# Kernel tuning notes

Hardware: AMD Instinct MI355X
Metric: run time of the kernel (lower is better)

Reference implementation:

```python
import jax, jax.numpy as jnp
import numpy as np

N = 8192
HID = 256
NCLS = 5
K = 10  # adj_parameter
IN_DIMS = [1000, 1000, 503]


def _leaky(x):
    return jnp.where(x >= 0, x, 0.25 * x)


def _batchnorm(x, g, b):
    # training-mode BatchNorm1d with batch stats (biased var), eps=1e-5
    mu = jnp.mean(x, axis=0)
    var = jnp.mean((x - mu) ** 2, axis=0)
    return (x - mu) * jax.lax.rsqrt(var + 1e-5) * g + b


def _build_adj(feat):
    # cosine similarity, per-row top-(K+1) (top-1 is self, diag=1), scatter,
    # add identity, L1 row-normalize. Vectorized equivalent of the torch loop.
    norm = jnp.maximum(jnp.linalg.norm(feat, axis=1, keepdims=True), 1e-12)
    fn = feat / norm
    sim = fn @ fn.T                                  # [N, N]
    vals, idx = jax.lax.top_k(sim, K + 1)            # [N, K+1]
    rows = jnp.arange(sim.shape[0])[:, None]
    adj = jnp.zeros_like(sim).at[rows, idx[:, 1:]].set(vals[:, 1:])
    adj = adj + jnp.eye(sim.shape[0], dtype=sim.dtype)
    rs = jnp.maximum(jnp.sum(jnp.abs(adj), axis=1, keepdims=True), 1e-12)
    return adj / rs


def setup_inputs() -> dict:
    key = jax.random.key(0)
    ks = jax.random.split(key, 24)
    d = {}
    d['x1'] = jax.random.normal(ks[0], (N, IN_DIMS[0]), jnp.float32)
    d['x2'] = jax.random.normal(ks[1], (N, IN_DIMS[1]), jnp.float32)
    d['x3'] = jax.random.normal(ks[2], (N, IN_DIMS[2]), jnp.float32)
    def xavier(k, shape):
        fan_in, fan_out = shape[-2], shape[-1]
        std = np.sqrt(2.0 / (fan_in + fan_out))
        return jax.random.normal(k, shape, jnp.float32) * std
    d['enc_W1'] = xavier(ks[3], (IN_DIMS[0], HID))
    d['enc_W2'] = xavier(ks[4], (IN_DIMS[1], HID))
    d['enc_W3'] = xavier(ks[5], (IN_DIMS[2], HID))
    d['enc_b'] = jnp.zeros((3, HID), jnp.float32)
    d['bn_g'] = jnp.ones((3, HID), jnp.float32)
    d['bn_b'] = jnp.zeros((3, HID), jnp.float32)
    d['gc1_W'] = xavier(ks[6], (3, HID, HID))
    d['gc1_b'] = jnp.zeros((3, HID), jnp.float32)
    d['gc2_W'] = xavier(ks[7], (3, HID, HID))
    d['gc2_b'] = jnp.zeros((3, HID), jnp.float32)
    d['clf_W'] = xavier(ks[8], (3, HID, NCLS))
    d['clf_b'] = jnp.zeros((3, NCLS), jnp.float32)
    d['attn'] = xavier(ks[9], (3, 1))[:, 0]
    d['f1_W'] = xavier(ks[10], (NCLS, 128))
    d['f1_b'] = jnp.zeros((128,), jnp.float32)
    d['f2_W'] = xavier(ks[11], (128, NCLS))
    d['f2_b'] = jnp.zeros((NCLS,), jnp.float32)
    return d


def reference(x1, x2, x3, enc_W1, enc_W2, enc_W3, enc_b, bn_g, bn_b,
              gc1_W, gc1_b, gc2_W, gc2_b, clf_W, clf_b,
              attn, f1_W, f1_b, f2_W, f2_b):
    xs = [x1, x2, x3]
    enc_Ws = [enc_W1, enc_W2, enc_W3]
    logits_list = []
    for i in range(3):
        # modal encoder: Linear -> ReLU -> BatchNorm (dropout off, eval)
        feat = jax.nn.relu(xs[i] @ enc_Ws[i] + enc_b[i])
        feat = _batchnorm(feat, bn_g[i], bn_b[i])
        adj = _build_adj(feat)
        # SimpleGCN: two GraphConvolution layers with leaky_relu(0.25)
        h = _leaky(adj @ (feat @ gc1_W[i]) + gc1_b[i])
        h = _leaky(adj @ (h @ gc2_W[i]) + gc2_b[i])
        logits_list.append(h @ clf_W[i] + clf_b[i])
    # SimpleVCDN fusion
    w = jax.nn.softmax(attn)
    fused = sum(w[i] * jax.nn.sigmoid(logits_list[i]) for i in range(3))
    out = _leaky(fused @ f1_W + f1_b) @ f2_W + f2_b
    return out
```

## Files before the change

### kernel.cpp

```cpp
#include <hip/hip_runtime.h>
#include <cfloat>
#include <cstdint>
#include <cstddef>

#define NROWS 8192
#define HID 256
#define NCLS 5
#define TOPK 10
#define CAP 256
#define TM 128
#define TN 128
#define BK 32
#define BKS 64

typedef __bf16 bf16x8 __attribute__((ext_vector_type(8)));
typedef float f32x4 __attribute__((ext_vector_type(4)));

__device__ inline ushort f2bf(float x) {
  unsigned u = __float_as_uint(x);
  unsigned r = (u + 0x7fffu + ((u >> 16) & 1u)) >> 16;
  return (ushort)r;
}
__device__ inline float bf2f(ushort b) { return __uint_as_float(((unsigned)b) << 16); }

__device__ __forceinline__ void load_lds16(const void* g, void* l) {
  __builtin_amdgcn_global_load_lds(
      (const __attribute__((address_space(1))) void*)g,
      (__attribute__((address_space(3))) void*)l, 16, 0, 0);
}

__global__ __launch_bounds__(256) void packAB_kernel(const float* __restrict__ X0,
    const float* __restrict__ X1, const float* __restrict__ X2,
    const float* __restrict__ W0, const float* __restrict__ W1,
    const float* __restrict__ W2, ushort* __restrict__ Ah, ushort* __restrict__ Al,
    ushort* __restrict__ Bh, ushort* __restrict__ Bl,
    int D0, int D1, int D2, int Kp0, int Kp1, int Kp2,
    size_t aOff0, size_t aOff1, size_t aOff2,
    size_t wOff0, size_t wOff1, size_t wOff2) {
  const int z = blockIdx.y;
  const float* X = (z == 0) ? X0 : (z == 1) ? X1 : X2;
  const float* W = (z == 0) ? W0 : (z == 1) ? W1 : W2;
  const int D = (z == 0) ? D0 : (z == 1) ? D1 : D2;
  const int Kp = (z == 0) ? Kp0 : (z == 1) ? Kp1 : Kp2;
  const size_t aOff = (z == 0) ? aOff0 : (z == 1) ? aOff1 : aOff2;
  const size_t wOff = (z == 0) ? wOff0 : (z == 1) ? wOff1 : wOff2;
  const int ksh = 31 - __clz(Kp);
  const int id = blockIdx.x * 256 + threadIdx.x;
  const int atotal = NROWS << ksh;
  if (id >= atotal + (HID << ksh)) return;
  if (id < atotal) {
    const int k = id & (Kp - 1);
    const int r = id >> ksh;
    const float x = (k < D) ? X[(size_t)r * D + k] : 0.f;
    const ushort h = f2bf(x);
    Ah[aOff + id] = h;
    Al[aOff + id] = f2bf(x - bf2f(h));
  } else {
    const int id2 = id - atotal;
    const int k = id2 & (Kp - 1);
    const int n = id2 >> ksh;
    const float x = (k < D) ? W[(size_t)k * HID + n] : 0.f;
    const ushort h = f2bf(x);
    Bh[wOff + id2] = h;
    Bl[wOff + id2] = f2bf(x - bf2f(h));
  }
}

__global__ __launch_bounds__(256) void packW_kernel(const float* __restrict__ W,
    ushort* __restrict__ Bh, ushort* __restrict__ Bl) {
  const int z = blockIdx.y;
  const int id = blockIdx.x * 256 + threadIdx.x;
  const int k = id >> 8, n = id & 255;
  const size_t wz = (size_t)z * HID * HID;
  const float x = W[wz + (size_t)k * HID + n];
  const ushort h = f2bf(x);
  Bh[wz + (size_t)n * HID + k] = h;
  Bl[wz + (size_t)n * HID + k] = f2bf(x - bf2f(h));
}

template<bool BIAS, int ACT>
__global__ __launch_bounds__(256) void limbgemm_kernel(const ushort* __restrict__ Ah,
    const ushort* __restrict__ Al, const ushort* __restrict__ Bh,
    const ushort* __restrict__ Bl, const float* __restrict__ bias,
    float* __restrict__ C, int Kp0, int Kp1, int Kp2,
    size_t aOff0, size_t aOff1, size_t aOff2,
    size_t bOff0, size_t bOff1, size_t bOff2) {
  __shared__ ushort AsH[TM * BK], AsL[TM * BK], BsH[TM * BK], BsL[TM * BK];
  const int z = blockIdx.y;
  const int Kp = (z == 0) ? Kp0 : (z == 1) ? Kp1 : Kp2;
  const size_t aO = (z == 0) ? aOff0 : (z == 1) ? aOff1 : aOff2;
  const size_t bO = (z == 0) ? bOff0 : (z == 1) ? bOff1 : bOff2;
  Ah += aO; Al += aO; Bh += bO; Bl += bO;
  C += (size_t)z * NROWS * HID;
  const int tid = threadIdx.x;
  const int wave = tid >> 6, lane = tid & 63;
  const int bid = blockIdx.x;
  const int xcd = bid & 7, slot = bid >> 3;
  const int bxi = slot & 1;
  const int byi = xcd * 8 + (slot >> 1);
  const int bm = byi * TM, bn = bxi * 128;
  const int wr = (wave >> 1) * 64, wc = (wave & 1) * 64;

  f32x4 acc[4][4];
  const f32x4 zero = {0.f, 0.f, 0.f, 0.f};
  #pragma unroll
  for (int i = 0; i < 4; ++i)
    #pragma unroll
    for (int j = 0; j < 4; ++j) acc[i][j] = zero;

  const int p0 = tid, p1 = tid + 256;
  const int r0 = p0 >> 2, kl0 = (p0 & 3) ^ ((r0 & 3) ^ ((r0 >> 2) & 1));
  const int r1 = p1 >> 2, kl1 = (p1 & 3) ^ ((r1 & 3) ^ ((r1 >> 2) & 1));
  const size_t a0 = (size_t)(bm + r0) * Kp + kl0 * 8;
  const size_t a1 = (size_t)(bm + r1) * Kp + kl1 * 8;
  const size_t b0 = (size_t)(bn + r0) * Kp + kl0 * 8;
  const size_t b1 = (size_t)(bn + r1) * Kp + kl1 * 8;

  for (int k0 = 0; k0 < Kp; k0 += BK) {
    __syncthreads();
    load_lds16(Ah + a0 + k0, &AsH[p0 * 8]);
    load_lds16(Ah + a1 + k0, &AsH[p1 * 8]);
    load_lds16(Al + a0 + k0, &AsL[p0 * 8]);
    load_lds16(Al + a1 + k0, &AsL[p1 * 8]);
    load_lds16(Bh + b0 + k0, &BsH[p0 * 8]);
    load_lds16(Bh + b1 + k0, &BsH[p1 * 8]);
    load_lds16(Bl + b0 + k0, &BsL[p0 * 8]);
    load_lds16(Bl + b1 + k0, &BsL[p1 * 8]);
    __syncthreads();
    bf16x8 ah[4], al[4], bh[4], bl[4];
    const int kg = lane >> 4;
    #pragma unroll
    for (int f = 0; f < 4; ++f) {
      const int m = wr + f * 16 + (lane & 15);
      const int sa = m * 4 + (kg ^ (m & 3) ^ ((m >> 2) & 1));
      ah[f] = *(const bf16x8*)&AsH[sa * 8];
      al[f] = *(const bf16x8*)&AsL[sa * 8];
      const int n = wc + f * 16 + (lane & 15);
      const int sb = n * 4 + (kg ^ (n & 3) ^ ((n >> 2) & 1));
      bh[f] = *(const bf16x8*)&BsH[sb * 8];
      bl[f] = *(const bf16x8*)&BsL[sb * 8];
    }
    #pragma unroll
    for (int fr = 0; fr < 4; ++fr)
      #pragma unroll
      for (int fc = 0; fc < 4; ++fc) {
        acc[fr][fc] = __builtin_amdgcn_mfma_f32_16x16x32_bf16(ah[fr], bh[fc], acc[fr][fc], 0, 0, 0);
        acc[fr][fc] = __builtin_amdgcn_mfma_f32_16x16x32_bf16(ah[fr], bl[fc], acc[fr][fc], 0, 0, 0);
        acc[fr][fc] = __builtin_amdgcn_mfma_f32_16x16x32_bf16(al[fr], bh[fc], acc[fr][fc], 0, 0, 0);
      }
  }
  const int cq = lane >> 4, cc = lane & 15;
  #pragma unroll
  for (int fr = 0; fr < 4; ++fr) {
    #pragma unroll
    for (int fc = 0; fc < 4; ++fc) {
      const int rb = bm + wr + fr * 16 + cq * 4;
      const int col = bn + wc + fc * 16 + cc;
      const float bb = BIAS ? bias[z * HID + col] : 0.f;
      float* cp = C + (size_t)rb * HID + col;
      #pragma unroll
      for (int e = 0; e < 4; ++e) {
        float v = acc[fr][fc][e] + bb;
        if (ACT == 1) v = fmaxf(v, 0.f);
        cp[(size_t)e * HID] = v;
      }
    }
  }
}

__global__ __launch_bounds__(256) void bn_stats_kernel(const float* __restrict__ F,
    float* __restrict__ ps, float* __restrict__ ps2) {
  const int z = blockIdx.y;
  const int b = blockIdx.x, t = threadIdx.x;
  float s = 0.f, s2 = 0.f;
  const float* p = F + (size_t)z * NROWS * HID + (size_t)b * 128 * HID + t;
  for (int r = 0; r < 128; ++r) {
    const float v = p[(size_t)r * HID];
    s += v; s2 += v * v;
  }
  ps[(size_t)z * 64 * HID + b * HID + t] = s;
  ps2[(size_t)z * 64 * HID + b * HID + t] = s2;
}

__global__ __launch_bounds__(256) void bn_finalize_kernel(const float* __restrict__ ps,
    const float* __restrict__ ps2, const float* __restrict__ g,
    const float* __restrict__ b, float* __restrict__ scale, float* __restrict__ shift) {
  const int z = blockIdx.x;
  const int t = threadIdx.x;
  float s = 0.f, s2 = 0.f;
  for (int i = 0; i < 64; ++i) {
    s += ps[(size_t)z * 64 * HID + i * HID + t];
    s2 += ps2[(size_t)z * 64 * HID + i * HID + t];
  }
  const float mu = s / (float)NROWS;
  const float var = s2 / (float)NROWS - mu * mu;
  const float rstd = rsqrtf(var + 1e-5f);
  const float sc = rstd * g[z * HID + t];
  scale[z * HID + t] = sc;
  shift[z * HID + t] = b[z * HID + t] - mu * sc;
}

__global__ __launch_bounds__(256) void bn_rownorm_kernel(const float* __restrict__ F,
    const float* __restrict__ scale, const float* __restrict__ shift,
    float* __restrict__ FN, ushort* __restrict__ Ph,
    ushort* __restrict__ Fh, ushort* __restrict__ Fl) {
  const int z = blockIdx.y;
  const int r = blockIdx.x, t = threadIdx.x;
  const size_t zb = (size_t)z * NROWS * HID;
  const float f = F[zb + (size_t)r * HID + t] * scale[z * HID + t] + shift[z * HID + t];
  __shared__ float sh[256];
  sh[t] = f * f;
  __syncthreads();
  for (int st = 128; st > 0; st >>= 1) {
    if (t < st) sh[t] += sh[t + st];
    __syncthreads();
  }
  const float inv = 1.0f / fmaxf(sqrtf(sh[0]), 1e-12f);
  const float fn = f * inv;
  const size_t o = zb + (size_t)r * HID + t;
  FN[o] = fn;
  Ph[o] = f2bf(fn);
  const ushort h = f2bf(f);
  Fh[o] = h;
  Fl[o] = f2bf(f - bf2f(h));
}

template<int PASS>
__global__ __launch_bounds__(512) void simtile_kernel(const ushort* __restrict__ P,
    float* __restrict__ M, const float* __restrict__ tauv,
    int* __restrict__ gcnt, int* __restrict__ gidx) {
  const int bx = blockIdx.x, by = blockIdx.y;
  if (by > bx) return;
  const int z = blockIdx.z;
  P += (size_t)z * NROWS * HID;
  if (PASS == 0) M += (size_t)z * NROWS * 64;
  else {
    tauv += (size_t)z * NROWS;
    gcnt += (size_t)z * NROWS;
    gidx += (size_t)z * NROWS * CAP;
  }
  const bool offdiag = (bx != by);
  __shared__ ushort As[TM * BKS];
  __shared__ ushort Bs[TN * BKS];
  __shared__ float Ml[2][TM];
  __shared__ float MlC[4][TN];
  __shared__ float taulA[TM];
  __shared__ float taulB[TN];
  const int tid = threadIdx.x;
  const int wave = tid >> 6, lane = tid & 63;
  const int bm = by * TM;
  const int bn = bx * TN;
  const int wr = (wave >> 1) * 32;
  const int wc = (wave & 1) * 64;

  if (PASS == 1) {
    if (tid < TM) taulA[tid] = tauv[bm + tid];
    else if (tid < TM + TN) taulB[tid - TM] = tauv[bn + (tid - TM)];
  }

  const ushort* pa[2];
  const ushort* pb[2];
  #pragma unroll
  for (int j = 0; j < 2; ++j) {
    const int s = tid + j * 512;
    const int m = s >> 3;
    const int kg = (s & 7) ^ (m & 7);
    pa[j] = P + (size_t)(bm + m) * HID + kg * 8;
    pb[j] = P + (size_t)(bn + m) * HID + kg * 8;
  }

  f32x4 acc[2][4];
  const f32x4 zero = {0.f, 0.f, 0.f, 0.f};
  #pragma unroll
  for (int i = 0; i < 2; ++i)
    #pragma unroll
    for (int j = 0; j < 4; ++j) acc[i][j] = zero;

  for (int k0 = 0; k0 < HID; k0 += BKS) {
    __syncthreads();
    #pragma unroll
    for (int j = 0; j < 2; ++j) {
      load_lds16(pa[j] + k0, &As[(tid + j * 512) * 8]);
      load_lds16(pb[j] + k0, &Bs[(tid + j * 512) * 8]);
    }
    __syncthreads();
    #pragma unroll
    for (int h = 0; h < 2; ++h) {
      const int kgb = h * 4 + (lane >> 4);
      bf16x8 af[2], bf[4];
      #pragma unroll
      for (int f = 0; f < 2; ++f) {
        const int m = wr + f * 16 + (lane & 15);
        const int sa = m * 8 + (kgb ^ (m & 7));
        af[f] = *(const bf16x8*)&As[sa * 8];
      }
      #pragma unroll
      for (int f = 0; f < 4; ++f) {
        const int n = wc + f * 16 + (lane & 15);
        const int sb = n * 8 + (kgb ^ (n & 7));
        bf[f] = *(const bf16x8*)&Bs[sb * 8];
      }
      #pragma unroll
      for (int fr = 0; fr < 2; ++fr)
        #pragma unroll
        for (int fc = 0; fc < 4; ++fc)
          acc[fr][fc] = __builtin_amdgcn_mfma_f32_16x16x32_bf16(af[fr], bf[fc], acc[fr][fc], 0, 0, 0);
    }
  }

  const int cq = lane >> 4, cc = lane & 15;
  if (PASS == 0) {
    #pragma unroll
    for (int fr = 0; fr < 2; ++fr) {
      #pragma unroll
      for (int e = 0; e < 4; ++e) {
        const int lrow = wr + fr * 16 + cq * 4 + e;
        const int grow = bm + lrow;
        float mx = -FLT_MAX;
        #pragma unroll
        for (int fc = 0; fc < 4; ++fc) {
          const int col = bn + wc + fc * 16 + cc;
          mx = fmaxf(mx, (col == grow) ? -FLT_MAX : acc[fr][fc][e]);
        }
        #pragma unroll
        for (int s = 1; s < 16; s <<= 1) mx = fmaxf(mx, __shfl_xor(mx, s));
        if (cc == 0) Ml[wave & 1][lrow] = mx;
      }
    }
    if (offdiag) {
      #pragma unroll
      for (int fc = 0; fc < 4; ++fc) {
        float mx = -FLT_MAX;
        #pragma unroll
        for (int fr = 0; fr < 2; ++fr)
          #pragma unroll
          for (int e = 0; e < 4; ++e) mx = fmaxf(mx, acc[fr][fc][e]);
        mx = fmaxf(mx, __shfl_xor(mx, 16));
        mx = fmaxf(mx, __shfl_xor(mx, 32));
        if (cq == 0) MlC[wave >> 1][wc + fc * 16 + cc] = mx;
      }
    }
    __syncthreads();
    if (tid < TM) M[(size_t)(bm + tid) * 64 + bx] = fmaxf(Ml[0][tid], Ml[1][tid]);
    if (offdiag && tid < TN) {
      const float mx = fmaxf(fmaxf(MlC[0][tid], MlC[1][tid]),
                             fmaxf(MlC[2][tid], MlC[3][tid]));
      M[(size_t)(bn + tid) * 64 + by] = mx;
    }
  } else {
    __syncthreads();
    #pragma unroll
    for (int fr = 0; fr < 2; ++fr) {
      #pragma unroll
      for (int e = 0; e < 4; ++e) {
        const int lrow = wr + fr * 16 + cq * 4 + e;
        const int grow = bm + lrow;
        const float tA = taulA[lrow];
        #pragma unroll
        for (int fc = 0; fc < 4; ++fc) {
          const int lcol = wc + fc * 16 + cc;
          const int gcol = bn + lcol;
          const float v = acc[fr][fc][e];
          if (gcol != grow && v >= tA) {
            const int pos = atomicAdd(&gcnt[grow], 1);
            if (pos < CAP) gidx[(size_t)grow * CAP + pos] = gcol;
          }
          if (offdiag && v >= taulB[lcol]) {
            const int pos = atomicAdd(&gcnt[gcol], 1);
            if (pos < CAP) gidx[(size_t)gcol * CAP + pos] = grow;
          }
        }
      }
    }
  }
}

__global__ __launch_bounds__(256) void tau_kernel(const float* __restrict__ M,
    float* __restrict__ tauv, int* __restrict__ gcnt) {
  const int z = blockIdx.y;
  const int wave = threadIdx.x >> 6, lane = threadIdx.x & 63;
  const int row = blockIdx.x * 4 + wave;
  float cur = M[(size_t)z * NROWS * 64 + (size_t)row * 64 + lane];
  float tau = cur;
  #pragma unroll
  for (int sel = 0; sel < 16; ++sel) {
    float bv = cur;
    int bl = lane;
    #pragma unroll
    for (int s = 1; s < 64; s <<= 1) {
      const float ov = __shfl_xor(bv, s);
      const int ol = __shfl_xor(bl, s);
      if (ov > bv || (ov == bv && ol < bl)) { bv = ov; bl = ol; }
    }
    tau = bv;
    if (lane == bl) cur = -FLT_MAX;
  }
  if (lane == 0) {
    tauv[(size_t)z * NROWS + row] = tau;
    gcnt[(size_t)z * NROWS + row] = 0;
  }
}

__global__ __launch_bounds__(256) void refine_kernel(const int* __restrict__ gcnt,
    const int* __restrict__ gidx, const float* __restrict__ FN,
    int* __restrict__ nidx, float* __restrict__ nval, float* __restrict__ dinv) {
  const int z = blockIdx.y;
  gcnt += (size_t)z * NROWS;
  gidx += (size_t)z * NROWS * CAP;
  FN += (size_t)z * NROWS * HID;
  nidx += (size_t)z * NROWS * TOPK;
  nval += (size_t)z * NROWS * TOPK;
  dinv += (size_t)z * NROWS;
  const int wave = threadIdx.x >> 6, lane = threadIdx.x & 63;
  const int row = blockIdx.x * 4 + wave;
  const int cnt = min(gcnt[row], CAP);
  __shared__ float fnrow[4][HID];
  __shared__ float ev[4][CAP];
  ((float4*)fnrow[wave])[lane] = ((const float4*)(FN + (size_t)row * HID))[lane];
  __syncthreads();
  const int c = lane >> 2, q4 = lane & 3;
  for (int b0 = 0; b0 < cnt; b0 += 16) {
    const int ci = b0 + c;
    const int cand = (ci < cnt) ? gidx[(size_t)row * CAP + ci] : 0;
    float s = 0.f;
    const float* fc = FN + (size_t)cand * HID + q4 * 64;
    const float* fr = fnrow[wave] + q4 * 64;
    #pragma unroll 8
    for (int k = 0; k < 64; ++k) s += fr[k] * fc[k];
    s += __shfl_xor(s, 1);
    s += __shfl_xor(s, 2);
    if (q4 == 0 && ci < cnt) ev[wave][ci] = s;
  }
  __syncthreads();
  float outv[TOPK];
  int outi[TOPK];
  float sum = 1.0f;
  #pragma unroll
  for (int sel = 0; sel < TOPK; ++sel) {
    float bv = -FLT_MAX;
    int bp = 0;
    #pragma unroll
    for (int j = 0; j < 4; ++j) {
      const int p = lane + j * 64;
      if (p < cnt) {
        const float v = ev[wave][p];
        if (v > bv) { bv = v; bp = p; }
      }
    }
    #pragma unroll
    for (int s = 1; s < 64; s <<= 1) {
      const float ov = __shfl_xor(bv, s);
      const int op = __shfl_xor(bp, s);
      if (ov > bv || (ov == bv && op < bp)) { bv = ov; bp = op; }
    }
    outv[sel] = bv;
    outi[sel] = bp;
    sum += fabsf(bv);
    if (lane == 0) ev[wave][bp] = -FLT_MAX;
  }
  if (lane == 0) {
    const float inv = 1.0f / fmaxf(sum, 1e-12f);
    dinv[row] = inv;
    #pragma unroll
    for (int sel = 0; sel < TOPK; ++sel) {
      nval[row * TOPK + sel] = outv[sel] * inv;
      nidx[row * TOPK + sel] = gidx[(size_t)row * CAP + outi[sel]];
    }
  }
}

template<int EMIT>
__global__ __launch_bounds__(256) void spmm_kernel(const float* __restrict__ T,
    const int* __restrict__ nidx, const float* __restrict__ nval,
    const float* __restrict__ dinv, const float* __restrict__ bias,
    ushort* __restrict__ Hh, ushort* __restrict__ Hl,
    const float* __restrict__ clfW, const float* __restrict__ clfb,
    float* __restrict__ L) {
  const int z = blockIdx.y;
  const size_t zb = (size_t)z * NROWS * HID;
  T += zb;
  nidx += (size_t)z * NROWS * TOPK;
  nval += (size_t)z * NROWS * TOPK;
  dinv += (size_t)z * NROWS;
  const int r = blockIdx.x, c = threadIdx.x;
  float acc = dinv[r] * T[(size_t)r * HID + c];
  #pragma unroll
  for (int n = 0; n < TOPK; ++n) {
    acc += nval[r * TOPK + n] * T[(size_t)nidx[r * TOPK + n] * HID + c];
  }
  acc += bias[z * HID + c];
  const float v = acc >= 0.f ? acc : 0.25f * acc;
  if (EMIT == 1) {
    const size_t o = zb + (size_t)r * HID + c;
    const ushort h = f2bf(v);
    Hh[o] = h;
    Hl[o] = f2bf(v - bf2f(h));
  } else {
    __shared__ float wsum[4][NCLS];
    const int wave = c >> 6, lane = c & 63;
    const float* wrow = clfW + (size_t)z * HID * NCLS + (size_t)c * NCLS;
    #pragma unroll
    for (int cls = 0; cls < NCLS; ++cls) {
      float p = v * wrow[cls];
      #pragma unroll
      for (int s = 1; s < 64; s <<= 1) p += __shfl_xor(p, s);
      if (lane == 0) wsum[wave][cls] = p;
    }
    __syncthreads();
    if (c < NCLS) {
      const float lg = clfb[z * NCLS + c] + wsum[0][c] + wsum[1][c] + wsum[2][c] + wsum[3][c];
      L[(size_t)z * NROWS * NCLS + (size_t)r * NCLS + c] = lg;
    }
  }
}

__global__ __launch_bounds__(256) void fuse_kernel(const float* __restrict__ L,
    const float* __restrict__ attn, float* __restrict__ fused) {
  const int id = blockIdx.x * 256 + threadIdx.x;
  if (id >= NROWS * NCLS) return;
  const float a0 = attn[0], a1 = attn[1], a2 = attn[2];
  const float m = fmaxf(a0, fmaxf(a1, a2));
  const float e0 = expf(a0 - m), e1 = expf(a1 - m), e2 = expf(a2 - m);
  const float inv = 1.0f / (e0 + e1 + e2);
  const float l0 = L[id];
  const float l1 = L[NROWS * NCLS + id];
  const float l2 = L[2 * NROWS * NCLS + id];
  const float s0 = 1.0f / (1.0f + expf(-l0));
  const float s1 = 1.0f / (1.0f + expf(-l1));
  const float s2 = 1.0f / (1.0f + expf(-l2));
  fused[id] = (e0 * s0 + e1 * s1 + e2 * s2) * inv;
}

__global__ __launch_bounds__(128) void head_kernel(const float* __restrict__ fused,
    const float* __restrict__ W1, const float* __restrict__ b1,
    const float* __restrict__ W2, const float* __restrict__ b2,
    float* __restrict__ out) {
  const int r = blockIdx.x, t = threadIdx.x;
  __shared__ float f[NCLS];
  __shared__ float hh[128];
  if (t < NCLS) f[t] = fused[r * NCLS + t];
  __syncthreads();
  float s = b1[t];
  #pragma unroll
  for (int k = 0; k < NCLS; ++k) s += f[k] * W1[k * 128 + t];
  hh[t] = s >= 0.f ? s : 0.25f * s;
  __syncthreads();
  if (t < NCLS) {
    float o = b2[t];
    for (int k = 0; k < 128; ++k) o += hh[k] * W2[k * NCLS + t];
    out[r * NCLS + t] = o;
  }
}

extern "C" void kernel_launch(void* const* d_in, const int* in_sizes, int n_in,
                              void* d_out, int out_size, void* d_ws, size_t ws_size,
                              hipStream_t stream) {
  const float* x0 = (const float*)d_in[0];
  const float* x1 = (const float*)d_in[1];
  const float* x2 = (const float*)d_in[2];
  const float* eW0 = (const float*)d_in[3];
  const float* eW1 = (const float*)d_in[4];
  const float* eW2 = (const float*)d_in[5];
  const float* enc_b = (const float*)d_in[6];
  const float* bn_g  = (const float*)d_in[7];
  const float* bn_b  = (const float*)d_in[8];
  const float* gc1W  = (const float*)d_in[9];
  const float* gc1b  = (const float*)d_in[10];
  const float* gc2W  = (const float*)d_in[11];
  const float* gc2b  = (const float*)d_in[12];
  const float* clfW  = (const float*)d_in[13];
  const float* clfb  = (const float*)d_in[14];
  const float* attn  = (const float*)d_in[15];
  const float* f1W   = (const float*)d_in[16];
  const float* f1b   = (const float*)d_in[17];
  const float* f2W   = (const float*)d_in[18];
  const float* f2b   = (const float*)d_in[19];
  float* out = (float*)d_out;

  int Kp[3];
  for (int m = 0; m < 3; ++m) {
    const int D = in_sizes[m] / NROWS;
    int k = 256;
    while (k < D) k <<= 1;
    Kp[m] = k;
  }
  const size_t KpSum = (size_t)Kp[0] + Kp[1] + Kp[2];
  const int D0 = in_sizes[0] / NROWS, D1 = in_sizes[1] / NROWS, D2 = in_sizes[2] / NROWS;

  const size_t NH = (size_t)NROWS * HID;
  float* ws = (float*)d_ws;
  float* A = ws;
  float* C = A;
  float* nval = A + 3 * NH;
  int*   nidx = (int*)(nval + (size_t)3 * NROWS * TOPK);
  float* dinv = (float*)(nidx + (size_t)3 * NROWS * TOPK);
  float* logits = dinv + 3 * NROWS;
  float* fused = logits + (size_t)3 * NROWS * NCLS;
  float* ps    = fused + (size_t)NROWS * NCLS;
  float* ps2   = ps + 3 * 64 * HID;
  float* scale = ps2 + 3 * 64 * HID;
  float* shift = scale + 3 * HID;
  float* M     = shift + 3 * HID;
  float* tauv  = M + (size_t)3 * NROWS * 64;
  int*   gcnt  = (int*)(tauv + 3 * NROWS);
  int*   gidx  = gcnt + 3 * NROWS;
  ushort* WhG = (ushort*)(gidx + (size_t)3 * NROWS * CAP);
  ushort* WlG = WhG + (size_t)3 * HID * HID;
  ushort* WhE = WlG + (size_t)3 * HID * HID;
  ushort* WlE = WhE + (size_t)HID * KpSum;
  char* u3 = (char*)(WlE + (size_t)HID * KpSum);
  float* FN = (float*)u3;
  ushort* Ph = (ushort*)(FN + 3 * NH);
  ushort* Fh = Ph + 3 * NH;
  ushort* Fl = Fh + 3 * NH;
  ushort* Hh = Fl + 3 * NH;
  ushort* Hl = Hh + 3 * NH;
  ushort* AhE = (ushort*)u3;
  ushort* AlE = AhE + (size_t)NROWS * KpSum;

  const size_t aOff0 = 0, aOff1 = (size_t)NROWS * Kp[0],
               aOff2 = (size_t)NROWS * (Kp[0] + Kp[1]);
  const size_t wOff0 = 0, wOff1 = (size_t)HID * Kp[0],
               wOff2 = (size_t)HID * (Kp[0] + Kp[1]);

  const dim3 blk(256);
  packAB_kernel<<<dim3(((NROWS + HID) * 1024) / 256, 3), blk, 0, stream>>>(
      x0, x1, x2, eW0, eW1, eW2, AhE, AlE, WhE, WlE,
      D0, D1, D2, Kp[0], Kp[1], Kp[2], aOff0, aOff1, aOff2, wOff0, wOff1, wOff2);
  limbgemm_kernel<true, 1><<<dim3(128, 3), blk, 0, stream>>>(
      AhE, AlE, WhE, WlE, enc_b, A, Kp[0], Kp[1], Kp[2],
      aOff0, aOff1, aOff2, wOff0, wOff1, wOff2);
  bn_stats_kernel<<<dim3(64, 3), blk, 0, stream>>>(A, ps, ps2);
  bn_finalize_kernel<<<3, blk, 0, stream>>>(ps, ps2, bn_g, bn_b, scale, shift);
  bn_rownorm_kernel<<<dim3(NROWS, 3), blk, 0, stream>>>(A, scale, shift, FN, Ph, Fh, Fl);
  simtile_kernel<0><<<dim3(64, 64, 3), dim3(512), 0, stream>>>(Ph, M, nullptr, nullptr, nullptr);
  tau_kernel<<<dim3(NROWS / 4, 3), blk, 0, stream>>>(M, tauv, gcnt);
  simtile_kernel<1><<<dim3(64, 64, 3), dim3(512), 0, stream>>>(Ph, nullptr, tauv, gcnt, gidx);
  refine_kernel<<<dim3(NROWS / 4, 3), blk, 0, stream>>>(gcnt, gidx, FN, nidx, nval, dinv);
  packW_kernel<<<dim3(256, 3), blk, 0, stream>>>(gc1W, WhG, WlG);
  limbgemm_kernel<false, 0><<<dim3(128, 3), blk, 0, stream>>>(
      Fh, Fl, WhG, WlG, nullptr, C, HID, HID, HID,
      0, NH, 2 * NH, 0, (size_t)HID * HID, (size_t)2 * HID * HID);
  spmm_kernel<1><<<dim3(NROWS, 3), blk, 0, stream>>>(C, nidx, nval, dinv, gc1b,
                                                     Hh, Hl, nullptr, nullptr, nullptr);
  packW_kernel<<<dim3(256, 3), blk, 0, stream>>>(gc2W, WhG, WlG);
  limbgemm_kernel<false, 0><<<dim3(128, 3), blk, 0, stream>>>(
      Hh, Hl, WhG, WlG, nullptr, C, HID, HID, HID,
      0, NH, 2 * NH, 0, (size_t)HID * HID, (size_t)2 * HID * HID);
  spmm_kernel<0><<<dim3(NROWS, 3), blk, 0, stream>>>(C, nidx, nval, dinv, gc2b,
                                                     nullptr, nullptr, clfW, clfb, logits);
  fuse_kernel<<<(NROWS * NCLS + 255) / 256, blk, 0, stream>>>(logits, attn, fused);
  head_kernel<<<NROWS, dim3(128), 0, stream>>>(fused, f1W, f1b, f2W, f2b, out);
}
```

Measured before the change: 838.5 us.

## Double-buffer LDS in GEMM kernels and launch only upper-triangular sim tiles

Both the limb GEMM and the similarity-tile kernel now keep two LDS buffers, so the next K-slab is fetched while the current one feeds the MFMAs, and each iteration needs one barrier instead of two. The similarity kernels are launched over a linear grid of 2080 triangular tiles, with bx/by recovered by a sqrt-based inverse, instead of a 64x64 grid where half the blocks exit at once. This doubles LDS use per block, which can lower occupancy, and the tile index decode adds a little integer work per block.

```diff
diff --git a/kernel.cpp b/kernel.cpp
--- a/kernel.cpp
+++ b/kernel.cpp
@@ -78,6 +78,16 @@
   Bl[wz + (size_t)n * HID + k] = f2bf(x - bf2f(h));
 }
 
+#define STAGE_LIMB(B, K0)                              \
+    load_lds16(Ah + a0 + (K0), &AsH[B][p0 * 8]);       \
+    load_lds16(Ah + a1 + (K0), &AsH[B][p1 * 8]);       \
+    load_lds16(Al + a0 + (K0), &AsL[B][p0 * 8]);       \
+    load_lds16(Al + a1 + (K0), &AsL[B][p1 * 8]);       \
+    load_lds16(Bh + b0 + (K0), &BsH[B][p0 * 8]);       \
+    load_lds16(Bh + b1 + (K0), &BsH[B][p1 * 8]);       \
+    load_lds16(Bl + b0 + (K0), &BsL[B][p0 * 8]);       \
+    load_lds16(Bl + b1 + (K0), &BsL[B][p1 * 8]);
+
 template<bool BIAS, int ACT>
 __global__ __launch_bounds__(256) void limbgemm_kernel(const ushort* __restrict__ Ah,
     const ushort* __restrict__ Al, const ushort* __restrict__ Bh,
@@ -85,7 +95,7 @@
     float* __restrict__ C, int Kp0, int Kp1, int Kp2,
     size_t aOff0, size_t aOff1, size_t aOff2,
     size_t bOff0, size_t bOff1, size_t bOff2) {
-  __shared__ ushort AsH[TM * BK], AsL[TM * BK], BsH[TM * BK], BsL[TM * BK];
+  __shared__ ushort AsH[2][TM * BK], AsL[2][TM * BK], BsH[2][TM * BK], BsL[2][TM * BK];
   const int z = blockIdx.y;
   const int Kp = (z == 0) ? Kp0 : (z == 1) ? Kp1 : Kp2;
   const size_t aO = (z == 0) ? aOff0 : (z == 1) ? aOff1 : aOff2;
@@ -116,29 +126,25 @@
   const size_t b0 = (size_t)(bn + r0) * Kp + kl0 * 8;
   const size_t b1 = (size_t)(bn + r1) * Kp + kl1 * 8;
 
+  STAGE_LIMB(0, 0)
+  __syncthreads();
+  int cur = 0;
   for (int k0 = 0; k0 < Kp; k0 += BK) {
-    __syncthreads();
-    load_lds16(Ah + a0 + k0, &AsH[p0 * 8]);
-    load_lds16(Ah + a1 + k0, &AsH[p1 * 8]);
-    load_lds16(Al + a0 + k0, &AsL[p0 * 8]);
-    load_lds16(Al + a1 + k0, &AsL[p1 * 8]);
-    load_lds16(Bh + b0 + k0, &BsH[p0 * 8]);
-    load_lds16(Bh + b1 + k0, &BsH[p1 * 8]);
-    load_lds16(Bl + b0 + k0, &BsL[p0 * 8]);
-    load_lds16(Bl + b1 + k0, &BsL[p1 * 8]);
-    __syncthreads();
+    if (k0 + BK < Kp) {
+      STAGE_LIMB(cur ^ 1, k0 + BK)
+    }
     bf16x8 ah[4], al[4], bh[4], bl[4];
     const int kg = lane >> 4;
     #pragma unroll
     for (int f = 0; f < 4; ++f) {
       const int m = wr + f * 16 + (lane & 15);
       const int sa = m * 4 + (kg ^ (m & 3) ^ ((m >> 2) & 1));
-      ah[f] = *(const bf16x8*)&AsH[sa * 8];
-      al[f] = *(const bf16x8*)&AsL[sa * 8];
+      ah[f] = *(const bf16x8*)&AsH[cur][sa * 8];
+      al[f] = *(const bf16x8*)&AsL[cur][sa * 8];
       const int n = wc + f * 16 + (lane & 15);
       const int sb = n * 4 + (kg ^ (n & 3) ^ ((n >> 2) & 1));
-      bh[f] = *(const bf16x8*)&BsH[sb * 8];
-      bl[f] = *(const bf16x8*)&BsL[sb * 8];
+      bh[f] = *(const bf16x8*)&BsH[cur][sb * 8];
+      bl[f] = *(const bf16x8*)&BsL[cur][sb * 8];
     }
     #pragma unroll
     for (int fr = 0; fr < 4; ++fr)
@@ -148,6 +154,8 @@
         acc[fr][fc] = __builtin_amdgcn_mfma_f32_16x16x32_bf16(ah[fr], bl[fc], acc[fr][fc], 0, 0, 0);
         acc[fr][fc] = __builtin_amdgcn_mfma_f32_16x16x32_bf16(al[fr], bh[fc], acc[fr][fc], 0, 0, 0);
       }
+    __syncthreads();
+    cur ^= 1;
   }
   const int cq = lane >> 4, cc = lane & 15;
   #pragma unroll
@@ -229,9 +237,12 @@
 __global__ __launch_bounds__(512) void simtile_kernel(const ushort* __restrict__ P,
     float* __restrict__ M, const float* __restrict__ tauv,
     int* __restrict__ gcnt, int* __restrict__ gidx) {
-  const int bx = blockIdx.x, by = blockIdx.y;
-  if (by > bx) return;
-  const int z = blockIdx.z;
+  const int tlin = blockIdx.x;
+  int bx = (int)((sqrtf(8.0f * (float)tlin + 1.0f) - 1.0f) * 0.5f);
+  while ((bx + 1) * (bx + 2) / 2 <= tlin) ++bx;
+  while (bx * (bx + 1) / 2 > tlin) --bx;
+  const int by = tlin - bx * (bx + 1) / 2;
+  const int z = blockIdx.y;
   P += (size_t)z * NROWS * HID;
   if (PASS == 0) M += (size_t)z * NROWS * 64;
   else {
@@ -240,8 +251,8 @@
     gidx += (size_t)z * NROWS * CAP;
   }
   const bool offdiag = (bx != by);
-  __shared__ ushort As[TM * BKS];
-  __shared__ ushort Bs[TN * BKS];
+  __shared__ ushort As[2][TM * BKS];
+  __shared__ ushort Bs[2][TN * BKS];
   __shared__ float Ml[2][TM];
   __shared__ float MlC[4][TN];
   __shared__ float taulA[TM];
@@ -276,36 +287,45 @@
     #pragma unroll
     for (int j = 0; j < 4; ++j) acc[i][j] = zero;
 
+  #pragma unroll
+  for (int j = 0; j < 2; ++j) {
+    load_lds16(pa[j], &As[0][(tid + j * 512) * 8]);
+    load_lds16(pb[j], &Bs[0][(tid + j * 512) * 8]);
+  }
+  __syncthreads();
+  int cur = 0;
   for (int k0 = 0; k0 < HID; k0 += BKS) {
-    __syncthreads();
-    #pragma unroll
-    for (int j = 0; j < 2; ++j) {
-      load_lds16(pa[j] + k0, &As[(tid + j * 512) * 8]);
-      load_lds16(pb[j] + k0, &Bs[(tid + j * 512) * 8]);
-    }
-    __syncthreads();
+    if (k0 + BKS < HID) {
+      #pragma unroll
+      for (int j = 0; j < 2; ++j) {
+        load_lds16(pa[j] + k0 + BKS, &As[cur ^ 1][(tid + j * 512) * 8]);
+        load_lds16(pb[j] + k0 + BKS, &Bs[cur ^ 1][(tid + j * 512) * 8]);
+      }
+    }
     #pragma unroll
     for (int h = 0; h < 2; ++h) {
       const int kgb = h * 4 + (lane >> 4);
-      bf16x8 af[2], bf[4];
+      bf16x8 af[2], bfv[4];
       #pragma unroll
       for (int f = 0; f < 2; ++f) {
         const int m = wr + f * 16 + (lane & 15);
         const int sa = m * 8 + (kgb ^ (m & 7));
-        af[f] = *(const bf16x8*)&As[sa * 8];
+        af[f] = *(const bf16x8*)&As[cur][sa * 8];
       }
       #pragma unroll
       for (int f = 0; f < 4; ++f) {
         const int n = wc + f * 16 + (lane & 15);
         const int sb = n * 8 + (kgb ^ (n & 7));
-        bf[f] = *(const bf16x8*)&Bs[sb * 8];
+        bfv[f] = *(const bf16x8*)&Bs[cur][sb * 8];
       }
       #pragma unroll
       for (int fr = 0; fr < 2; ++fr)
         #pragma unroll
         for (int fc = 0; fc < 4; ++fc)
-          acc[fr][fc] = __builtin_amdgcn_mfma_f32_16x16x32_bf16(af[fr], bf[fc], acc[fr][fc], 0, 0, 0);
-    }
+          acc[fr][fc] = __builtin_amdgcn_mfma_f32_16x16x32_bf16(af[fr], bfv[fc], acc[fr][fc], 0, 0, 0);
+    }
+    __syncthreads();
+    cur ^= 1;
   }
 
   const int cq = lane >> 4, cc = lane & 15;
@@ -633,9 +653,9 @@
   bn_stats_kernel<<<dim3(64, 3), blk, 0, stream>>>(A, ps, ps2);
   bn_finalize_kernel<<<3, blk, 0, stream>>>(ps, ps2, bn_g, bn_b, scale, shift);
   bn_rownorm_kernel<<<dim3(NROWS, 3), blk, 0, stream>>>(A, scale, shift, FN, Ph, Fh, Fl);
-  simtile_kernel<0><<<dim3(64, 64, 3), dim3(512), 0, stream>>>(Ph, M, nullptr, nullptr, nullptr);
+  simtile_kernel<0><<<dim3(2080, 3), dim3(512), 0, stream>>>(Ph, M, nullptr, nullptr, nullptr);
   tau_kernel<<<dim3(NROWS / 4, 3), blk, 0, stream>>>(M, tauv, gcnt);
-  simtile_kernel<1><<<dim3(64, 64, 3), dim3(512), 0, stream>>>(Ph, nullptr, tauv, gcnt, gidx);
+  simtile_kernel<1><<<dim3(2080, 3), dim3(512), 0, stream>>>(Ph, nullptr, tauv, gcnt, gidx);
   refine_kernel<<<dim3(NROWS / 4, 3), blk, 0, stream>>>(gcnt, gidx, FN, nidx, nval, dinv);
   packW_kernel<<<dim3(256, 3), blk, 0, stream>>>(gc1W, WhG, WlG);
   limbgemm_kernel<false, 0><<<dim3(128, 3), blk, 0, stream>>>(
```

New measurement: 813.6 us. 1.03x faster.
